# Performance work log

Measured on AMD Instinct MI355X. Metric: run time of the kernel, lower is better.

Reference implementation:

```python
import jax, jax.numpy as jnp
import numpy as np

H = 512      # LSTM hidden size (hard-coded in BiLstm)
ATT = 20     # attention size
EPS = 1e-5


def _ln(x, gamma, beta):
    mu = x.mean(-1, keepdims=True)
    var = x.var(-1, keepdims=True)
    return (x - mu) / jnp.sqrt(var + EPS) * gamma + beta


def _bn(x, gamma, beta):
    # BatchNorm1d in training mode: x [B, C, T], stats over (batch, time)
    mu = x.mean((0, 2), keepdims=True)
    var = x.var((0, 2), keepdims=True)
    return (x - mu) / jnp.sqrt(var + EPS) * gamma[None, :, None] + beta[None, :, None]


def _lstm_dir(x_seq, w_ih, w_hh, g_gamma, g_beta, c_gamma, c_beta, reverse):
    # x_seq: [T, B, in] ; w_ih: [4H, in] ; w_hh: [4H, H]
    T, B, _ = x_seq.shape
    xp = jnp.einsum('tbi,gi->tbg', x_seq, w_ih)  # precompute input projections [T,B,4H]
    gg = g_gamma.reshape(4, H)
    gb = g_beta.reshape(4, H)

    def step(carry, xt):
        h, c = carry
        pre = xt + h @ w_hh.T                    # [B, 4H]
        pre = _ln(pre.reshape(B, 4, H), gg, gb)  # per-gate LayerNorm
        i, f, g, o = pre[:, 0], pre[:, 1], pre[:, 2], pre[:, 3]
        c = jax.nn.sigmoid(f) * c + jax.nn.sigmoid(i) * jnp.tanh(g)
        h = jax.nn.sigmoid(o) * jnp.tanh(_ln(c, c_gamma, c_beta))
        return (h, c), h

    init = (jnp.zeros((B, H), x_seq.dtype), jnp.zeros((B, H), x_seq.dtype))
    _, hs = jax.lax.scan(step, init, xp, reverse=reverse)
    return hs  # [T, B, H], time-ordered


def _bilstm_layer(x_seq, w_ih, w_hh, gg, gb, cg, cb):
    fwd = _lstm_dir(x_seq, w_ih[0], w_hh[0], gg[0], gb[0], cg[0], cb[0], False)
    bwd = _lstm_dir(x_seq, w_ih[1], w_hh[1], gg[1], gb[1], cg[1], cb[1], True)
    return jnp.concatenate([fwd, bwd], axis=-1)  # [T, B, 2H]


def setup_inputs() -> dict:
    key = jax.random.key(0)
    ks = jax.random.split(key, 12)
    B, T, V = 32, 512, 128
    d = {}
    d['x'] = jax.random.normal(ks[0], (B, T, V), jnp.float32)
    # BatchNorm params
    d['bn1_gamma'] = jnp.ones((V,), jnp.float32)
    d['bn1_beta'] = jnp.zeros((V,), jnp.float32)
    d['bn2_gamma'] = jnp.ones((2 * H,), jnp.float32)
    d['bn2_beta'] = jnp.zeros((2 * H,), jnp.float32)
    # Layer 0 (input V), layer 1 (input 2H); 2 directions stacked on axis 0
    d['w_ih0'] = jax.random.normal(ks[1], (2, 4 * H, V), jnp.float32) * 0.05
    d['w_hh0'] = jax.random.normal(ks[2], (2, 4 * H, H), jnp.float32) * 0.05
    d['g_gamma0'] = jnp.ones((2, 4 * H), jnp.float32)
    d['g_beta0'] = jnp.zeros((2, 4 * H), jnp.float32)
    d['c_gamma0'] = jnp.ones((2, H), jnp.float32)
    d['c_beta0'] = jnp.zeros((2, H), jnp.float32)
    d['w_ih1'] = jax.random.normal(ks[3], (2, 4 * H, 2 * H), jnp.float32) * 0.05
    d['w_hh1'] = jax.random.normal(ks[4], (2, 4 * H, H), jnp.float32) * 0.05
    d['g_gamma1'] = jnp.ones((2, 4 * H), jnp.float32)
    d['g_beta1'] = jnp.zeros((2, 4 * H), jnp.float32)
    d['c_gamma1'] = jnp.ones((2, H), jnp.float32)
    d['c_beta1'] = jnp.zeros((2, H), jnp.float32)
    # Attention params
    d['w_omega'] = jax.random.normal(ks[5], (2 * H, ATT), jnp.float32) * 0.05
    d['b_omega'] = jax.random.normal(ks[6], (ATT,), jnp.float32) * 0.05
    d['u_omega'] = jax.random.normal(ks[7], (ATT,), jnp.float32) * 0.05
    return d


def reference(x, bn1_gamma, bn1_beta, bn2_gamma, bn2_beta,
              w_ih0, w_hh0, g_gamma0, g_beta0, c_gamma0, c_beta0,
              w_ih1, w_hh1, g_gamma1, g_beta1, c_gamma1, c_beta1,
              w_omega, b_omega, u_omega):
    # x: [B, T, V]; dropout layers are identity (eval)
    h = jnp.transpose(x, (0, 2, 1))              # [B, V, T]
    h = _bn(h, bn1_gamma, bn1_beta)
    h = jnp.transpose(h, (2, 0, 1))              # [T, B, V]
    h = _bilstm_layer(h, w_ih0, w_hh0, g_gamma0, g_beta0, c_gamma0, c_beta0)
    h = _bilstm_layer(h, w_ih1, w_hh1, g_gamma1, g_beta1, c_gamma1, c_beta1)
    h = jnp.transpose(h, (1, 2, 0))              # [B, 2H, T]
    h = _bn(h, bn2_gamma, bn2_beta)
    h = jnp.transpose(h, (0, 2, 1))              # [B, T, 2H]
    # Additive attention pooling
    v = jnp.tanh(h @ w_omega + b_omega)          # [B, T, ATT]
    vu = v @ u_omega                             # [B, T]
    alphas = jax.nn.softmax(vu, axis=1)
    out = jnp.sum(h * alphas[..., None], axis=1)  # [B, 2H]
    return out
```

## Files before the change

kernel.cpp:

```cpp
#include <hip/hip_runtime.h>
#include <hip/hip_bf16.h>

#define LN_EPS 1e-5f

typedef __attribute__((ext_vector_type(4))) float    f32x4;
typedef __attribute__((ext_vector_type(8))) _Float16 f16x8;
typedef __attribute__((ext_vector_type(4))) unsigned u32x4;

__device__ __forceinline__ float fsig(float x){
  return 1.0f/(1.0f + __expf(-x));
}
__device__ __forceinline__ float ftanh(float x){
  float xx = fminf(fmaxf(x, -15.f), 15.f);
  float e = __expf(2.f*xx);
  return (e - 1.f)/(e + 1.f);
}

__device__ __forceinline__ float agent_load_f(const float* p){
  return __hip_atomic_load((float*)p, __ATOMIC_RELAXED, __HIP_MEMORY_SCOPE_AGENT);
}
__device__ __forceinline__ void agent_store_f(float* p, float v){
  __hip_atomic_store(p, v, __ATOMIC_RELAXED, __HIP_MEMORY_SCOPE_AGENT);
}

__global__ void k_bn1_stats(const float* __restrict__ x, float* __restrict__ stats){
  int tid = threadIdx.x;
  int cg = tid >> 3, ro = tid & 7;
  int c4 = cg * 4;
  float s[4] = {0,0,0,0}, q[4] = {0,0,0,0};
  int rbase = blockIdx.x * 64;
  for (int i = 0; i < 8; ++i){
    int row = rbase + i*8 + ro;
    f32x4 v = *(const f32x4*)(x + (size_t)row*128 + c4);
    #pragma unroll
    for (int e=0;e<4;e++){ s[e]+=v[e]; q[e]+=v[e]*v[e]; }
  }
  #pragma unroll
  for (int o=1;o<8;o<<=1){
    #pragma unroll
    for (int e=0;e<4;e++){ s[e]+=__shfl_xor(s[e],o); q[e]+=__shfl_xor(q[e],o); }
  }
  if (ro==0){
    #pragma unroll
    for (int e=0;e<4;e++){
      atomicAdd(&stats[c4+e], s[e]);
      atomicAdd(&stats[128+c4+e], q[e]);
    }
  }
}

__global__ void k_bn1_fin(const float* __restrict__ stats, const float* __restrict__ gamma,
                          const float* __restrict__ beta, float* __restrict__ ss){
  int c = threadIdx.x;
  if (c < 128){
    float N = 16384.0f;
    float mean = stats[c]/N;
    float var  = stats[128+c]/N - mean*mean;
    float scale = gamma[c] * rsqrtf(var + LN_EPS);
    ss[c] = scale;
    ss[128+c] = beta[c] - mean*scale;
  }
}

__global__ void k_cvt_f16(const float* __restrict__ s, _Float16* __restrict__ d, int n){
  for (int i = blockIdx.x*blockDim.x + threadIdx.x; i < n; i += gridDim.x*blockDim.x)
    d[i] = (_Float16)s[i];
}

__global__ void k_pack_whh(const float* __restrict__ whh, _Float16* __restrict__ wpk){
  size_t i = (size_t)blockIdx.x*256 + threadIdx.x;
  int k = (int)(i & 511);
  size_t ci = i >> 9;
  int col = (int)(ci & 2047);
  int dirr = (int)(ci >> 11);
  int gate = col >> 9, cig = col & 511, c16 = cig >> 4, lc = cig & 15;
  int kt = k >> 5, ksub = k & 31, hi = ksub >> 3, j = ksub & 7;
  size_t dst = ((((size_t)(dirr*4+gate)*16 + kt)*32 + c16)*64 + (hi*16+lc))*8 + j;
  wpk[dst] = (_Float16)whh[i];
}

__global__ __launch_bounds__(256) void gemm_f16(const float* __restrict__ A,
                                                const _Float16* __restrict__ Bp,
                                                _Float16* __restrict__ C,
                                                int M, int N, int K,
                                                int a_mode, const float* __restrict__ ss){
  __shared__ __align__(16) _Float16 As[128*32];
  __shared__ __align__(16) _Float16 Bs[128*32];
  int n0 = blockIdx.x * 128, m0 = blockIdx.y * 128;
  int tid = threadIdx.x, lane = tid & 63, wave = tid >> 6;
  int wm = wave >> 1, wn = wave & 1;
  f32x4 acc[4][4] = {};
  int r = tid >> 2, sseg = tid & 3;
  for (int kt = 0; kt < K; kt += 32){
    #pragma unroll
    for (int half = 0; half < 2; ++half){
      int m = m0 + half*64 + r;
      const float* src;
      if (a_mode){
        int t = m >> 5, b = m & 31;
        src = A + ((size_t)(b*512 + t))*128 + kt + sseg*8;
      } else {
        src = A + (size_t)m*K + kt + sseg*8;
      }
      f32x4 v0 = *(const f32x4*)src;
      f32x4 v1 = *(const f32x4*)(src + 4);
      f16x8 vh;
      #pragma unroll
      for (int e=0;e<4;e++){
        float f0 = v0[e], f1 = v1[e];
        if (a_mode){
          int k = kt + sseg*8;
          f0 = f0*ss[k+e]   + ss[128+k+e];
          f1 = f1*ss[k+4+e] + ss[128+k+4+e];
        }
        vh[e] = (_Float16)f0; vh[4+e] = (_Float16)f1;
      }
      *(f16x8*)&As[(half*64+r)*32 + sseg*8] = vh;
      u32x4 bv = *(const u32x4*)(Bp + (size_t)(n0 + half*64 + r)*K + kt + sseg*8);
      *(u32x4*)&Bs[(half*64+r)*32 + sseg*8] = bv;
    }
    __syncthreads();
    f16x8 af[4], bf[4];
    int k8 = (lane >> 4) * 8;
    int ra = wm*64 + (lane & 15), rb = wn*64 + (lane & 15);
    #pragma unroll
    for (int mi=0;mi<4;mi++) af[mi] = *(const f16x8*)&As[(ra + mi*16)*32 + k8];
    #pragma unroll
    for (int ni=0;ni<4;ni++) bf[ni] = *(const f16x8*)&Bs[(rb + ni*16)*32 + k8];
    #pragma unroll
    for (int mi=0;mi<4;mi++)
      #pragma unroll
      for (int ni=0;ni<4;ni++)
        acc[mi][ni] = __builtin_amdgcn_mfma_f32_16x16x32_f16(af[mi], bf[ni], acc[mi][ni], 0, 0, 0);
    __syncthreads();
  }
  #pragma unroll
  for (int mi=0;mi<4;mi++)
    #pragma unroll
    for (int ni=0;ni<4;ni++){
      int col  = n0 + wn*64 + ni*16 + (lane & 15);
      int row0 = m0 + wm*64 + mi*16 + (lane >> 4)*4;
      #pragma unroll
      for (int rr=0;rr<4;rr++)
        C[(size_t)(row0+rr)*N + col] = (_Float16)acc[mi][ni][rr];
    }
}

#define CHUNK 516

__global__ __launch_bounds__(512, 1) void lstm_fast(
    const _Float16* __restrict__ xp,
    const _Float16* __restrict__ wpk,
    const float* __restrict__ gg, const float* __restrict__ gb,
    const float* __restrict__ cgam, const float* __restrict__ cbet,
    float* __restrict__ out,
    float* __restrict__ tf,
    unsigned* __restrict__ flags)
{
  int blk = blockIdx.x;
  int sub = blk & 15;
  int bq = blk >> 4;
  int dir = sub >> 3, gate = (sub >> 1) & 3, half = sub & 1;
  int tid = threadIdx.x, lane = tid & 63, wv = tid >> 6;
  int b0 = bq * 2;
  int grp = bq*2 + dir;
  int blkbase = (bq << 4) | (dir << 3);
  int own_sub = gate*2 + half;

  __shared__ __align__(16) _Float16 hfrag[16*64*8];
  __shared__ float c_s[2][512];
  __shared__ float red[8][2][2];
  __shared__ float redc[8][2][2];

  for (int i = tid; i < 16*64*8; i += 512) hfrag[i] = (_Float16)0.f;
  for (int i = tid; i < 2*512;  i += 512) c_s[i>>9][i&511] = 0.f;
  __syncthreads();

  int j = tid;
  float g0s = gg[dir*2048 + j],        g0b = gb[dir*2048 + j];
  float g1s = gg[dir*2048 + 512 + j],  g1b = gb[dir*2048 + 512 + j];
  float g2s = gg[dir*2048 + 1024 + j], g2b = gb[dir*2048 + 1024 + j];
  float g3s = gg[dir*2048 + 1536 + j], g3b = gb[dir*2048 + 1536 + j];
  float cgv = cgam[dir*512 + j],       cbv = cbet[dir*512 + j];

  const _Float16* wbase = wpk + (size_t)(dir*4 + gate) * (16*32*64*8);
  int c16a = half*16 + wv*2, c16b = c16a + 1;
  f16x8 wA[16], wB[16];
  #pragma unroll
  for (int kt = 0; kt < 16; ++kt){
    wA[kt] = *(const f16x8*)&wbase[(((size_t)kt*32 + c16a)*64 + lane)*8];
    wB[kt] = *(const f16x8*)&wbase[(((size_t)kt*32 + c16b)*64 + lane)*8];
  }

  for (int t = 0; t < 512; ++t){
    asm volatile("" : "+v"(wA[0]), "+v"(wA[1]), "+v"(wA[2]), "+v"(wA[3]),
                      "+v"(wA[4]), "+v"(wA[5]), "+v"(wA[6]), "+v"(wA[7]));
    asm volatile("" : "+v"(wA[8]), "+v"(wA[9]), "+v"(wA[10]), "+v"(wA[11]),
                      "+v"(wA[12]), "+v"(wA[13]), "+v"(wA[14]), "+v"(wA[15]));
    asm volatile("" : "+v"(wB[0]), "+v"(wB[1]), "+v"(wB[2]), "+v"(wB[3]),
                      "+v"(wB[4]), "+v"(wB[5]), "+v"(wB[6]), "+v"(wB[7]));
    asm volatile("" : "+v"(wB[8]), "+v"(wB[9]), "+v"(wB[10]), "+v"(wB[11]),
                      "+v"(wB[12]), "+v"(wB[13]), "+v"(wB[14]), "+v"(wB[15]));
    int pos = dir ? (511 - t) : t;
    int buf = t & 1;
    float xv0[2], xv1[2];
    if (lane < 16){
      const _Float16* xb = xp + (size_t)(pos*32 + b0)*4096 + dir*2048 + gate*512 + half*256;
      #pragma unroll
      for (int r = 0; r < 2; ++r){
        xv0[r] = (float)xb[(size_t)r*4096 + (wv*2)*16 + lane];
        xv1[r] = (float)xb[(size_t)r*4096 + (wv*2)*16 + lane + 16];
      }
    }
    f32x4 acc0 = {}, acc1 = {};
    #pragma unroll
    for (int kt = 0; kt < 16; ++kt){
      f16x8 afrag = *(const f16x8*)&hfrag[(kt*64 + lane)*8];
      acc0 = __builtin_amdgcn_mfma_f32_16x16x32_f16(afrag, wA[kt], acc0, 0, 0, 0);
      acc1 = __builtin_amdgcn_mfma_f32_16x16x32_f16(afrag, wB[kt], acc1, 0, 0, 0);
    }
    float* chk = tf + ((size_t)(grp*2 + buf)*8 + own_sub)*CHUNK;
    float s[2] = {0,0}, q[2] = {0,0};
    if (lane < 16){
      int cA = (wv*2)*16 + lane, cB = cA + 16;
      #pragma unroll
      for (int r = 0; r < 2; ++r){
        float v0 = acc0[r] + xv0[r];
        float v1 = acc1[r] + xv1[r];
        agent_store_f(chk + r*256 + cA, v0);
        agent_store_f(chk + r*256 + cB, v1);
        s[r] = v0 + v1; q[r] = v0*v0 + v1*v1;
      }
    }
    #pragma unroll
    for (int o = 1; o < 16; o <<= 1){
      #pragma unroll
      for (int r = 0; r < 2; ++r){ s[r] += __shfl_xor(s[r], o); q[r] += __shfl_xor(q[r], o); }
    }
    if (lane == 0){
      #pragma unroll
      for (int r = 0; r < 2; ++r){ red[wv][r][0] = s[r]; red[wv][r][1] = q[r]; }
    }
    __syncthreads();
    if (tid < 4){
      int b = tid >> 1, wh = tid & 1;
      float S = 0.f;
      #pragma unroll
      for (int w8 = 0; w8 < 8; ++w8) S += red[w8][b][wh];
      agent_store_f(chk + 512 + b*2 + wh, S);
    }
    asm volatile("s_waitcnt vmcnt(0)" ::: "memory");
    if (lane == 0)
      __hip_atomic_fetch_add(&flags[blk*64], 1u, __ATOMIC_RELAXED, __HIP_MEMORY_SCOPE_AGENT);
    if (tid < 7){
      int idx = tid < own_sub ? tid : tid + 1;
      int sblk = blkbase + idx;
      while (__hip_atomic_load(&flags[sblk*64], __ATOMIC_RELAXED, __HIP_MEMORY_SCOPE_AGENT)
             < (unsigned)(8*(t+1))){ }
    }
    __syncthreads();
    const float* gbase = tf + ((size_t)(grp*2 + buf)*8)*CHUNK;
    int hf = j >> 8, cc = j & 255;
    float p[4][2];
    #pragma unroll
    for (int g = 0; g < 4; ++g){
      const float* cp = gbase + (size_t)(g*2 + hf)*CHUNK + cc;
      #pragma unroll
      for (int b = 0; b < 2; ++b) p[g][b] = agent_load_f(cp + b*256);
    }
    float mu[4][2], rs[4][2];
    #pragma unroll
    for (int g = 0; g < 4; ++g)
      #pragma unroll
      for (int b = 0; b < 2; ++b){
        float S = agent_load_f(gbase + (size_t)(g*2+0)*CHUNK + 512 + b*2)
                + agent_load_f(gbase + (size_t)(g*2+1)*CHUNK + 512 + b*2);
        float Q = agent_load_f(gbase + (size_t)(g*2+0)*CHUNK + 512 + b*2 + 1)
                + agent_load_f(gbase + (size_t)(g*2+1)*CHUNK + 512 + b*2 + 1);
        float mean = S*(1.0f/512.0f);
        float var  = Q*(1.0f/512.0f) - mean*mean;
        mu[g][b] = mean; rs[g][b] = rsqrtf(var + LN_EPS);
      }
    float cs[2], cq2[2], ov[2], cnv[2];
    #pragma unroll
    for (int b = 0; b < 2; ++b){
      float pi = (p[0][b] - mu[0][b])*rs[0][b]*g0s + g0b;
      float pf = (p[1][b] - mu[1][b])*rs[1][b]*g1s + g1b;
      float pv = (p[2][b] - mu[2][b])*rs[2][b]*g2s + g2b;
      ov[b]    = (p[3][b] - mu[3][b])*rs[3][b]*g3s + g3b;
      float cn = fsig(pf)*c_s[b][j] + fsig(pi)*ftanh(pv);
      c_s[b][j] = cn; cnv[b] = cn;
      cs[b] = cn; cq2[b] = cn*cn;
    }
    #pragma unroll
    for (int o = 1; o < 64; o <<= 1){
      #pragma unroll
      for (int b = 0; b < 2; ++b){ cs[b] += __shfl_xor(cs[b], o); cq2[b] += __shfl_xor(cq2[b], o); }
    }
    if (lane == 0){
      #pragma unroll
      for (int b = 0; b < 2; ++b){ redc[wv][b][0] = cs[b]; redc[wv][b][1] = cq2[b]; }
    }
    __syncthreads();
    #pragma unroll
    for (int b = 0; b < 2; ++b){
      float S = 0.f, Q = 0.f;
      #pragma unroll
      for (int w8 = 0; w8 < 8; ++w8){ S += redc[w8][b][0]; Q += redc[w8][b][1]; }
      float mean = S*(1.0f/512.0f);
      float var  = Q*(1.0f/512.0f) - mean*mean;
      float rstd = rsqrtf(var + LN_EPS);
      float cl = (cnv[b] - mean)*rstd*cgv + cbv;
      float hv = fsig(ov[b]) * ftanh(cl);
      hfrag[(((j >> 5)*64) + ((j & 31) >> 3)*16 + b)*8 + (j & 7)] = (_Float16)hv;
      if (own_sub == 0)
        out[(size_t)(pos*32 + b0 + b)*1024 + dir*512 + j] = hv;
    }
    __syncthreads();
  }
}

__global__ void k_bn2_stats(const float* __restrict__ h1, float* __restrict__ stats){
  int tid = threadIdx.x;
  int c4 = tid*4;
  float s[4]={0,0,0,0}, q[4]={0,0,0,0};
  int rbase = blockIdx.x*64;
  for (int i=0;i<64;i++){
    f32x4 v = *(const f32x4*)(h1 + (size_t)(rbase+i)*1024 + c4);
    #pragma unroll
    for (int e=0;e<4;e++){ s[e]+=v[e]; q[e]+=v[e]*v[e]; }
  }
  #pragma unroll
  for (int e=0;e<4;e++){
    atomicAdd(&stats[c4+e], s[e]);
    atomicAdd(&stats[1024+c4+e], q[e]);
  }
}

__global__ void k_bn2_fin(const float* __restrict__ stats, const float* __restrict__ gamma,
                          const float* __restrict__ beta, float* __restrict__ ss){
  int c = blockIdx.x*256 + threadIdx.x;
  if (c < 1024){
    float N = 16384.0f;
    float mean = stats[c]/N;
    float var  = stats[1024+c]/N - mean*mean;
    float scale = gamma[c] * rsqrtf(var + LN_EPS);
    ss[c] = scale;
    ss[1024+c] = beta[c] - mean*scale;
  }
}

__global__ void k_att1(const float* __restrict__ h1, const float* __restrict__ ss,
                       const float* __restrict__ wom, const float* __restrict__ bom,
                       const float* __restrict__ uom, float* __restrict__ vu){
  __shared__ float tmp[4][64];
  int tid = threadIdx.x, wave = tid >> 6, ln = tid & 63;
  int part = ln/20, a = ln - part*20;
  bool active = (part < 3);
  for (int rr = 0; rr < 4; ++rr){
    int row = blockIdx.x*16 + wave*4 + rr;
    float acc = 0.0f;
    if (active){
      int n0 = part*342, n1 = (part==2) ? 1024 : (n0+342);
      for (int n = n0; n < n1; ++n){
        float hv = h1[(size_t)row*1024 + n]*ss[n] + ss[1024+n];
        acc += hv * wom[n*20 + a];
      }
    }
    tmp[wave][ln] = acc;
    __syncthreads();
    float pv = 0.0f;
    if (ln < 20){
      float v = tanhf(tmp[wave][ln] + tmp[wave][ln+20] + tmp[wave][ln+40] + bom[ln]);
      pv = v*uom[ln];
    }
    #pragma unroll
    for (int o=1;o<32;o<<=1) pv += __shfl_xor(pv, o);
    if (ln == 0) vu[row] = pv;
    __syncthreads();
  }
}

__global__ void k_att3(const float* __restrict__ h1, const float* __restrict__ ss,
                       const float* __restrict__ vu, float* __restrict__ out){
  __shared__ float al[512];
  __shared__ float red[4];
  int tid = threadIdx.x;
  int b = blockIdx.x >> 3, ch = blockIdx.x & 7;
  for (int t = tid; t < 512; t += 128) al[t] = vu[t*32 + b];
  __syncthreads();
  float m = -1e30f;
  for (int t = tid; t < 512; t += 128) m = fmaxf(m, al[t]);
  #pragma unroll
  for (int o=1;o<64;o<<=1) m = fmaxf(m, __shfl_xor(m,o));
  if ((tid & 63) == 0) red[tid>>6] = m;
  __syncthreads();
  m = fmaxf(red[0], red[1]);
  float s = 0.0f;
  for (int t = tid; t < 512; t += 128){ float e = expf(al[t]-m); al[t] = e; s += e; }
  #pragma unroll
  for (int o=1;o<64;o<<=1) s += __shfl_xor(s,o);
  if ((tid & 63) == 0) red[2 + (tid>>6)] = s;
  __syncthreads();
  float inv = 1.0f / (red[2] + red[3]);
  int n = ch*128 + tid;
  float acc = 0.0f;
  #pragma unroll 4
  for (int t = 0; t < 512; ++t) acc += al[t]*h1[(size_t)(t*32+b)*1024 + n];
  out[b*1024 + n] = acc*inv*ss[n] + ss[1024+n];
}

extern "C" void kernel_launch(void* const* d_in, const int* in_sizes, int n_in,
                              void* d_out, int out_size, void* d_ws, size_t ws_size,
                              hipStream_t stream){
  const float* x    = (const float*)d_in[0];
  const float* bn1g = (const float*)d_in[1];
  const float* bn1b = (const float*)d_in[2];
  const float* bn2g = (const float*)d_in[3];
  const float* bn2b = (const float*)d_in[4];
  const float* wih0 = (const float*)d_in[5];
  const float* whh0 = (const float*)d_in[6];
  const float* gg0  = (const float*)d_in[7];
  const float* gb0  = (const float*)d_in[8];
  const float* cg0  = (const float*)d_in[9];
  const float* cb0  = (const float*)d_in[10];
  const float* wih1 = (const float*)d_in[11];
  const float* whh1 = (const float*)d_in[12];
  const float* gg1  = (const float*)d_in[13];
  const float* gb1  = (const float*)d_in[14];
  const float* cg1  = (const float*)d_in[15];
  const float* cb1  = (const float*)d_in[16];
  const float* wom  = (const float*)d_in[17];
  const float* bom  = (const float*)d_in[18];
  const float* uom  = (const float*)d_in[19];
  float* out = (float*)d_out;

  char* w = (char*)d_ws;
  size_t off = 0;
  auto take = [&](size_t bytes)->void*{
    void* p = w + off;
    off += (bytes + 255) & ~(size_t)255;
    return p;
  };
  _Float16* xp = (_Float16*)take(16384ull*4096*2);
  float* hA = (float*)take(16384ull*1024*4);
  _Float16* w0h = (_Float16*)take(4096ull*128*2);
  _Float16* w1h = (_Float16*)take(4096ull*1024*2);
  _Float16* wpk0 = (_Float16*)take(2ull*2048*512*2);
  _Float16* wpk1 = (_Float16*)take(2ull*2048*512*2);
  float* tilesf = (float*)take(32ull*2*8*CHUNK*4);
  unsigned* flags = (unsigned*)take(256ull*64*4);
  float* stats1 = (float*)take(256*4);
  float* ss1    = (float*)take(256*4);
  float* stats2 = (float*)take(2048*4);
  float* ss2    = (float*)take(2048*4);
  float* vu     = (float*)take(16384ull*4);
  (void)ws_size; (void)in_sizes; (void)n_in; (void)out_size;

  hipMemsetAsync(stats1, 0, 256*4, stream);
  hipMemsetAsync(stats2, 0, 2048*4, stream);

  k_bn1_stats<<<256,256,0,stream>>>(x, stats1);
  k_bn1_fin<<<1,128,0,stream>>>(stats1, bn1g, bn1b, ss1);
  k_cvt_f16<<<256,256,0,stream>>>(wih0, w0h, 4096*128);
  k_cvt_f16<<<2048,256,0,stream>>>(wih1, w1h, 4096*1024);
  k_pack_whh<<<8192,256,0,stream>>>(whh0, wpk0);
  k_pack_whh<<<8192,256,0,stream>>>(whh1, wpk1);

  gemm_f16<<<dim3(32,128),256,0,stream>>>(x, w0h, xp, 16384, 4096, 128, 1, ss1);

  hipMemsetAsync(flags, 0, 256*64*4, stream);
  lstm_fast<<<256,512,0,stream>>>(xp, wpk0, gg0, gb0, cg0, cb0, hA, tilesf, flags);

  gemm_f16<<<dim3(32,128),256,0,stream>>>(hA, w1h, xp, 16384, 4096, 1024, 0, nullptr);

  hipMemsetAsync(flags, 0, 256*64*4, stream);
  lstm_fast<<<256,512,0,stream>>>(xp, wpk1, gg1, gb1, cg1, cb1, hA, tilesf, flags);

  k_bn2_stats<<<256,256,0,stream>>>(hA, stats2);
  k_bn2_fin<<<4,256,0,stream>>>(stats2, bn2g, bn2b, ss2);
  k_att1<<<1024,256,0,stream>>>(hA, ss2, wom, bom, uom, vu);
  k_att3<<<256,128,0,stream>>>(hA, ss2, vu, out);
}
```

Measured before the change: 5.923 ms.

## Use block-level flag store and share gate LN stats via LDS

Each block now signals step completion with one plain store of the step counter after a block barrier, instead of every wave atomically incrementing the flag. Pollers compare against t+1 accordingly. The per-gate LayerNorm statistics are loaded from global memory by eight threads and broadcast through shared memory, instead of every thread issuing 32 redundant agent-scope loads. This cuts atomic traffic and global load pressure on the recurrent critical path, at the cost of two extra __syncthreads per timestep.

```diff
diff --git a/kernel.cpp b/kernel.cpp
--- a/kernel.cpp
+++ b/kernel.cpp
@@ -171,6 +171,7 @@
   __shared__ float c_s[2][512];
   __shared__ float red[8][2][2];
   __shared__ float redc[8][2][2];
+  __shared__ float lnstat[8][2];
 
   for (int i = tid; i < 16*64*8; i += 512) hfrag[i] = (_Float16)0.f;
   for (int i = tid; i < 2*512;  i += 512) c_s[i>>9][i&511] = 0.f;
@@ -250,13 +251,14 @@
       agent_store_f(chk + 512 + b*2 + wh, S);
     }
     asm volatile("s_waitcnt vmcnt(0)" ::: "memory");
-    if (lane == 0)
-      __hip_atomic_fetch_add(&flags[blk*64], 1u, __ATOMIC_RELAXED, __HIP_MEMORY_SCOPE_AGENT);
+    __syncthreads();
+    if (tid == 0)
+      __hip_atomic_store(&flags[blk*64], (unsigned)(t+1), __ATOMIC_RELAXED, __HIP_MEMORY_SCOPE_AGENT);
     if (tid < 7){
       int idx = tid < own_sub ? tid : tid + 1;
       int sblk = blkbase + idx;
       while (__hip_atomic_load(&flags[sblk*64], __ATOMIC_RELAXED, __HIP_MEMORY_SCOPE_AGENT)
-             < (unsigned)(8*(t+1))){ }
+             < (unsigned)(t+1)){ }
     }
     __syncthreads();
     const float* gbase = tf + ((size_t)(grp*2 + buf)*8)*CHUNK;
@@ -268,26 +270,26 @@
       #pragma unroll
       for (int b = 0; b < 2; ++b) p[g][b] = agent_load_f(cp + b*256);
     }
-    float mu[4][2], rs[4][2];
-    #pragma unroll
-    for (int g = 0; g < 4; ++g)
-      #pragma unroll
-      for (int b = 0; b < 2; ++b){
-        float S = agent_load_f(gbase + (size_t)(g*2+0)*CHUNK + 512 + b*2)
-                + agent_load_f(gbase + (size_t)(g*2+1)*CHUNK + 512 + b*2);
-        float Q = agent_load_f(gbase + (size_t)(g*2+0)*CHUNK + 512 + b*2 + 1)
-                + agent_load_f(gbase + (size_t)(g*2+1)*CHUNK + 512 + b*2 + 1);
-        float mean = S*(1.0f/512.0f);
-        float var  = Q*(1.0f/512.0f) - mean*mean;
-        mu[g][b] = mean; rs[g][b] = rsqrtf(var + LN_EPS);
-      }
+    if (tid < 8){
+      int g = tid >> 1, b = tid & 1;
+      float S = 0.f, Q = 0.f;
+      #pragma unroll
+      for (int hh = 0; hh < 2; ++hh){
+        S += agent_load_f(gbase + (size_t)(g*2 + hh)*CHUNK + 512 + b*2);
+        Q += agent_load_f(gbase + (size_t)(g*2 + hh)*CHUNK + 512 + b*2 + 1);
+      }
+      float mean = S*(1.0f/512.0f);
+      float var  = Q*(1.0f/512.0f) - mean*mean;
+      lnstat[tid][0] = mean; lnstat[tid][1] = rsqrtf(var + LN_EPS);
+    }
+    __syncthreads();
     float cs[2], cq2[2], ov[2], cnv[2];
     #pragma unroll
     for (int b = 0; b < 2; ++b){
-      float pi = (p[0][b] - mu[0][b])*rs[0][b]*g0s + g0b;
-      float pf = (p[1][b] - mu[1][b])*rs[1][b]*g1s + g1b;
-      float pv = (p[2][b] - mu[2][b])*rs[2][b]*g2s + g2b;
-      ov[b]    = (p[3][b] - mu[3][b])*rs[3][b]*g3s + g3b;
+      float pi = (p[0][b] - lnstat[0*2+b][0])*lnstat[0*2+b][1]*g0s + g0b;
+      float pf = (p[1][b] - lnstat[1*2+b][0])*lnstat[1*2+b][1]*g1s + g1b;
+      float pv = (p[2][b] - lnstat[2*2+b][0])*lnstat[2*2+b][1]*g2s + g2b;
+      ov[b]    = (p[3][b] - lnstat[3*2+b][0])*lnstat[3*2+b][1]*g3s + g3b;
       float cn = fsig(pf)*c_s[b][j] + fsig(pi)*ftanh(pv);
       c_s[b][j] = cn; cnv[b] = cn;
       cs[b] = cn; cq2[b] = cn*cn;
```

Measured after the change: 5.417 ms (median of 2 runs). 8.5% less time.
